# Performance work log

Hardware: AMD Instinct MI355X
Metric: run time of the kernel (lower is better)

## Reference

```python
import jax, jax.numpy as jnp
import numpy as np

S, B, D, A = 8192, 64, 512, 256


def setup_inputs() -> dict:
    key = jax.random.key(0)
    ks = jax.random.split(key, 7)
    return {
        "x": jax.random.normal(ks[0], (S, B, D), dtype=jnp.float32),
        "h": jax.random.normal(ks[1], (1, B, D), dtype=jnp.float32),
        "Wx": jax.random.normal(ks[2], (A, D), dtype=jnp.float32) * (1.0 / np.sqrt(D)),
        "bx": jax.random.normal(ks[3], (A,), dtype=jnp.float32) * 0.01,
        "Wh": jax.random.normal(ks[4], (A, D), dtype=jnp.float32) * (1.0 / np.sqrt(D)),
        "Wt": jax.random.normal(ks[5], (1, A), dtype=jnp.float32) * (1.0 / np.sqrt(A)),
        "bt": jax.random.normal(ks[6], (1,), dtype=jnp.float32) * 0.01,
    }


def reference(x, h, Wx, bx, Wh, Wt, bt):
    # x: (S, B, D) seq-first; h: (1, B, D) hidden state.
    # All Conv1d ops have kernel size 1 -> plain per-position matmuls.
    xb = jnp.transpose(x, (1, 0, 2))               # (B, S, D)
    wx = jnp.einsum('bsd,ad->bas', xb, Wx) + bx[None, :, None]   # (B, A, S)
    h0 = h.transpose(1, 0, 2).reshape(-1, h.shape[-1])           # (B, D)
    wh = h0 @ Wh.T                                                # (B, A)
    # score conv (A -> 1) on tanh(wx + wh), then softmax over seq dim
    score = jnp.einsum('a,bas->bs', Wt[0], jnp.tanh(wx + wh[:, :, None])) + bt[0]  # (B, S)
    attn = jax.nn.softmax(score, axis=-1)                         # (B, S)
    out = jnp.einsum('bs,bsd->bd', attn, xb)                      # (B, D)
    return out
```

## Files before the change

### kernel.cpp

```cpp
#include <hip/hip_runtime.h>


#define S_DIM 8192
#define B_DIM 64
#define D_DIM 512
#define A_DIM 256
#define BM 32
#define NTILES 256

typedef _Float16 half8 __attribute__((ext_vector_type(8)));
typedef float f32x4 __attribute__((ext_vector_type(4)));

__device__ __forceinline__ float tanh_fast(float x) {
  float e = __expf(2.0f * x);
  return 1.0f - 2.0f * __builtin_amdgcn_rcpf(e + 1.0f);
}

__global__ void __launch_bounds__(256)
convw_kernel(const float* __restrict__ Wx, _Float16* __restrict__ Wp) {
  const int idx = (blockIdx.x * 256 + threadIdx.x) * 8;
  const int a = idx >> 9;
  const int k = idx & 511;
  f32x4 va = *(const f32x4*)(Wx + idx);
  f32x4 vb = *(const f32x4*)(Wx + idx + 4);
  half8 hx;
#pragma unroll
  for (int i = 0; i < 4; ++i) { hx[i] = (_Float16)va[i]; hx[4 + i] = (_Float16)vb[i]; }
  const int ta = a >> 4, fr = a & 15;
  const int tk = k >> 5, fg = (k >> 3) & 3;
  *(half8*)(Wp + (ta * 16 + tk) * 512 + (fg * 16 + fr) * 8) = hx;
}

__global__ void __launch_bounds__(256)
whb_kernel(const float* __restrict__ h, const float* __restrict__ Wh,
           const float* __restrict__ bx, float* __restrict__ whb) {
  __shared__ float hs[D_DIM];
  const int b = blockIdx.x, tid = threadIdx.x;
  hs[tid] = h[b * D_DIM + tid];
  hs[tid + 256] = h[b * D_DIM + 256 + tid];
  __syncthreads();
  const int g = tid >> 4, i = tid & 15;
  for (int pass = 0; pass < 16; ++pass) {
    const int a = pass * 16 + g;
    const f32x4* wrow = (const f32x4*)(Wh + (size_t)a * D_DIM);
    float dot = 0.f;
#pragma unroll
    for (int k = 0; k < 8; ++k) {
      f32x4 wv = wrow[i + k * 16];
      f32x4 hv = *(const f32x4*)(hs + (i + k * 16) * 4);
      dot += wv[0] * hv[0] + wv[1] * hv[1] + wv[2] * hv[2] + wv[3] * hv[3];
    }
#pragma unroll
    for (int mask = 1; mask < 16; mask <<= 1) dot += __shfl_xor(dot, mask, 64);
    if (i == 0) whb[b * A_DIM + a] = dot + bx[a];
  }
}

__global__ void __launch_bounds__(256, 4)
paa_main(const float* __restrict__ x, const _Float16* __restrict__ Wp,
         const float* __restrict__ whb, const float* __restrict__ Wt,
         float* __restrict__ m_arr, float* __restrict__ l_arr,
         float* __restrict__ acc_arr) {
  __shared__ _Float16 xs[BM * D_DIM];
  __shared__ float scorep[4 * BM];

  const int tid = threadIdx.x;
  const int lane = tid & 63;
  const int wv = tid >> 6;
  const int b = blockIdx.x;
  const int tile = blockIdx.y;

  const int fr = lane & 15, fg = lane >> 4;
  const int akey = fr & 7;
  const _Float16* wp = Wp + wv * (4 * 16 * 512) + lane * 8;

  float wt_a[4], whb_a[4];
#pragma unroll
  for (int nf = 0; nf < 4; ++nf) {
    wt_a[nf]  = Wt[wv * 64 + nf * 16 + fr];
    whb_a[nf] = whb[b * A_DIM + wv * 64 + nf * 16 + fr];
  }

  const int srow = tid >> 3, sseg = tid & 7;
  const int skey = srow & 7;
  {
    const float* rp = x + ((size_t)(tile * BM + srow) * B_DIM + b) * D_DIM;
    f32x4 sa[4], sb[4];
#pragma unroll
    for (int p = 0; p < 4; ++p) {
      sa[p] = *(const f32x4*)(rp + p * 64 + sseg * 8);
      sb[p] = *(const f32x4*)(rp + p * 64 + sseg * 8 + 4);
    }
#pragma unroll
    for (int p = 0; p < 4; ++p) {
      half8 hx;
#pragma unroll
      for (int j = 0; j < 4; ++j) { hx[j] = (_Float16)sa[p][j]; hx[4 + j] = (_Float16)sb[p][j]; }
      const int ch = p * 8 + sseg;
      *(half8*)(xs + srow * D_DIM + ((ch ^ skey) * 8)) = hx;
    }
#pragma unroll
    for (int p = 0; p < 4; ++p) {
      sa[p] = *(const f32x4*)(rp + (4 + p) * 64 + sseg * 8);
      sb[p] = *(const f32x4*)(rp + (4 + p) * 64 + sseg * 8 + 4);
    }
#pragma unroll
    for (int p = 0; p < 4; ++p) {
      half8 hx;
#pragma unroll
      for (int j = 0; j < 4; ++j) { hx[j] = (_Float16)sa[p][j]; hx[4 + j] = (_Float16)sb[p][j]; }
      const int ch = (4 + p) * 8 + sseg;
      *(half8*)(xs + srow * D_DIM + ((ch ^ skey) * 8)) = hx;
    }
  }
  __syncthreads();

  f32x4 acc[2][4];
#pragma unroll
  for (int mi = 0; mi < 2; ++mi)
#pragma unroll
    for (int nf = 0; nf < 4; ++nf) acc[mi][nf] = (f32x4){0.f, 0.f, 0.f, 0.f};
#pragma unroll
  for (int tk = 0; tk < 16; ++tk) {
    const int slot = ((tk * 4 + fg) ^ akey) * 8;
    half8 af0 = *(const half8*)(xs + (fr) * D_DIM + slot);
    half8 af1 = *(const half8*)(xs + (16 + fr) * D_DIM + slot);
    half8 bf0 = *(const half8*)(wp + (0 * 16 + tk) * 512);
    half8 bf1 = *(const half8*)(wp + (1 * 16 + tk) * 512);
    half8 bf2 = *(const half8*)(wp + (2 * 16 + tk) * 512);
    half8 bf3 = *(const half8*)(wp + (3 * 16 + tk) * 512);
    acc[0][0] = __builtin_amdgcn_mfma_f32_16x16x32_f16(af0, bf0, acc[0][0], 0, 0, 0);
    acc[0][1] = __builtin_amdgcn_mfma_f32_16x16x32_f16(af0, bf1, acc[0][1], 0, 0, 0);
    acc[0][2] = __builtin_amdgcn_mfma_f32_16x16x32_f16(af0, bf2, acc[0][2], 0, 0, 0);
    acc[0][3] = __builtin_amdgcn_mfma_f32_16x16x32_f16(af0, bf3, acc[0][3], 0, 0, 0);
    acc[1][0] = __builtin_amdgcn_mfma_f32_16x16x32_f16(af1, bf0, acc[1][0], 0, 0, 0);
    acc[1][1] = __builtin_amdgcn_mfma_f32_16x16x32_f16(af1, bf1, acc[1][1], 0, 0, 0);
    acc[1][2] = __builtin_amdgcn_mfma_f32_16x16x32_f16(af1, bf2, acc[1][2], 0, 0, 0);
    acc[1][3] = __builtin_amdgcn_mfma_f32_16x16x32_f16(af1, bf3, acc[1][3], 0, 0, 0);
  }

  {
    float part[2][4];
#pragma unroll
    for (int mi = 0; mi < 2; ++mi)
#pragma unroll
      for (int r = 0; r < 4; ++r) part[mi][r] = 0.f;
#pragma unroll
    for (int nf = 0; nf < 4; ++nf)
#pragma unroll
      for (int mi = 0; mi < 2; ++mi)
#pragma unroll
        for (int r = 0; r < 4; ++r)
          part[mi][r] += wt_a[nf] * tanh_fast(acc[mi][nf][r] + whb_a[nf]);
#pragma unroll
    for (int mask = 1; mask < 16; mask <<= 1)
#pragma unroll
      for (int mi = 0; mi < 2; ++mi)
#pragma unroll
        for (int r = 0; r < 4; ++r) part[mi][r] += __shfl_xor(part[mi][r], mask, 64);
    if (fr == 0) {
#pragma unroll
      for (int mi = 0; mi < 2; ++mi)
#pragma unroll
        for (int r = 0; r < 4; ++r)
          scorep[wv * BM + mi * 16 + fg * 4 + r] = part[mi][r];
    }
  }
  __syncthreads();

  const int rl = lane & 31;
  float sv = scorep[rl] + scorep[BM + rl] + scorep[2 * BM + rl] + scorep[3 * BM + rl];
  float m = sv;
#pragma unroll
  for (int mask = 1; mask < 32; mask <<= 1) m = fmaxf(m, __shfl_xor(m, mask, 64));
  float p = __expf(sv - m);
  float lsum = p;
#pragma unroll
  for (int mask = 1; mask < 32; mask <<= 1) lsum += __shfl_xor(lsum, mask, 64);
  if (tid == 0) {
    m_arr[b * NTILES + tile] = m;
    l_arr[b * NTILES + tile] = lsum;
  }

  {
    const int q = lane >> 4;
    const int ch = wv * 16 + (lane & 15);
    float wacc[8];
#pragma unroll
    for (int j = 0; j < 8; ++j) wacc[j] = 0.f;
#pragma unroll
    for (int k = 0; k < 8; ++k) {
      const int row = q * 8 + k;
      const float pr = __shfl(p, row, 64);
      half8 xv = *(const half8*)(xs + row * D_DIM + ((ch ^ (row & 7)) * 8));
#pragma unroll
      for (int j = 0; j < 8; ++j) wacc[j] += pr * (float)xv[j];
    }
#pragma unroll
    for (int j = 0; j < 8; ++j) wacc[j] += __shfl_xor(wacc[j], 16, 64);
#pragma unroll
    for (int j = 0; j < 8; ++j) wacc[j] += __shfl_xor(wacc[j], 32, 64);
    if (lane < 16) {
      float* ob = acc_arr + ((size_t)(b * NTILES + tile)) * D_DIM + ch * 8;
      *(f32x4*)(ob) = (f32x4){wacc[0], wacc[1], wacc[2], wacc[3]};
      *(f32x4*)(ob + 4) = (f32x4){wacc[4], wacc[5], wacc[6], wacc[7]};
    }
  }
}

__global__ void __launch_bounds__(512)
combine_kernel(const float* __restrict__ m_arr, const float* __restrict__ l_arr,
               const float* __restrict__ acc_arr, float* __restrict__ out) {
  __shared__ float ml[NTILES], ls[NTILES], wl[NTILES];
  const int b = blockIdx.x, tid = threadIdx.x;
  if (tid < NTILES) {
    ml[tid] = m_arr[b * NTILES + tid];
    ls[tid] = l_arr[b * NTILES + tid];
  }
  __syncthreads();
  float M = -1e30f;
  for (int i = 0; i < NTILES; ++i) M = fmaxf(M, ml[i]);
  if (tid < NTILES) wl[tid] = __expf(ml[tid] - M);
  __syncthreads();
  float L = 0.f;
  for (int i = 0; i < NTILES; ++i) L += wl[i] * ls[i];
  float sum = 0.f;
  const size_t base = (size_t)b * NTILES * D_DIM + tid;
  for (int i = 0; i < NTILES; ++i) sum += wl[i] * acc_arr[base + (size_t)i * D_DIM];
  out[b * D_DIM + tid] = sum / L;
}

extern "C" void kernel_launch(void* const* d_in, const int* in_sizes, int n_in,
                              void* d_out, int out_size, void* d_ws, size_t ws_size,
                              hipStream_t stream) {
  const float* x = (const float*)d_in[0];
  const float* h = (const float*)d_in[1];
  const float* Wx = (const float*)d_in[2];
  const float* bx = (const float*)d_in[3];
  const float* Wh = (const float*)d_in[4];
  const float* Wt = (const float*)d_in[5];

  char* ws = (char*)d_ws;
  _Float16* Wp = (_Float16*)ws;
  float* whb = (float*)(ws + 262144);
  float* m_arr = (float*)(ws + 262144 + 65536);
  float* l_arr = (float*)(ws + 262144 + 65536 + 65536);
  float* acc_arr = (float*)(ws + 262144 + 3 * 65536);

  hipLaunchKernelGGL(convw_kernel, dim3(64), dim3(256), 0, stream, Wx, Wp);
  hipLaunchKernelGGL(whb_kernel, dim3(B_DIM), dim3(256), 0, stream, h, Wh, bx, whb);
  hipLaunchKernelGGL(paa_main, dim3(B_DIM, NTILES), dim3(256), 0, stream,
                     x, Wp, whb, Wt, m_arr, l_arr, acc_arr);
  hipLaunchKernelGGL(combine_kernel, dim3(B_DIM), dim3(512), 0, stream,
                     m_arr, l_arr, acc_arr, (float*)d_out);
}
```

Baseline: 368.0 us.

## Use 512-thread blocks with 8 waves and register-preloaded weight fragments

Doubles the main kernel's block size to 8 waves. Each wave now owns 32 of the 256 attention channels, and the x-tile load and weighted-sum phases are split across twice as many threads. All of the wave's Wp fragments (32 half8 values) are loaded into registers before the shared-memory sync, so weight fetch overlaps the x staging and the global loads leave the MFMA loop. This targets more memory parallelism and better latency hiding per block, at the cost of higher register pressure under launch_bounds(512, 8) and an extra shuffle stage in the reduction.

```diff
diff --git a/kernel.cpp b/kernel.cpp
--- a/kernel.cpp
+++ b/kernel.cpp
@@ -56,13 +56,13 @@
   }
 }
 
-__global__ void __launch_bounds__(256, 4)
+__global__ void __launch_bounds__(512, 8)
 paa_main(const float* __restrict__ x, const _Float16* __restrict__ Wp,
          const float* __restrict__ whb, const float* __restrict__ Wt,
          float* __restrict__ m_arr, float* __restrict__ l_arr,
          float* __restrict__ acc_arr) {
   __shared__ _Float16 xs[BM * D_DIM];
-  __shared__ float scorep[4 * BM];
+  __shared__ float scorep[8 * BM];
 
   const int tid = threadIdx.x;
   const int lane = tid & 63;
@@ -72,104 +72,90 @@
 
   const int fr = lane & 15, fg = lane >> 4;
   const int akey = fr & 7;
-  const _Float16* wp = Wp + wv * (4 * 16 * 512) + lane * 8;
-
-  float wt_a[4], whb_a[4];
-#pragma unroll
-  for (int nf = 0; nf < 4; ++nf) {
-    wt_a[nf]  = Wt[wv * 64 + nf * 16 + fr];
-    whb_a[nf] = whb[b * A_DIM + wv * 64 + nf * 16 + fr];
-  }
-
-  const int srow = tid >> 3, sseg = tid & 7;
+
+  const int srow = tid >> 4, sseg = tid & 15;
   const int skey = srow & 7;
-  {
-    const float* rp = x + ((size_t)(tile * BM + srow) * B_DIM + b) * D_DIM;
-    f32x4 sa[4], sb[4];
-#pragma unroll
-    for (int p = 0; p < 4; ++p) {
-      sa[p] = *(const f32x4*)(rp + p * 64 + sseg * 8);
-      sb[p] = *(const f32x4*)(rp + p * 64 + sseg * 8 + 4);
-    }
-#pragma unroll
-    for (int p = 0; p < 4; ++p) {
-      half8 hx;
-#pragma unroll
-      for (int j = 0; j < 4; ++j) { hx[j] = (_Float16)sa[p][j]; hx[4 + j] = (_Float16)sb[p][j]; }
-      const int ch = p * 8 + sseg;
-      *(half8*)(xs + srow * D_DIM + ((ch ^ skey) * 8)) = hx;
-    }
-#pragma unroll
-    for (int p = 0; p < 4; ++p) {
-      sa[p] = *(const f32x4*)(rp + (4 + p) * 64 + sseg * 8);
-      sb[p] = *(const f32x4*)(rp + (4 + p) * 64 + sseg * 8 + 4);
-    }
-#pragma unroll
-    for (int p = 0; p < 4; ++p) {
-      half8 hx;
-#pragma unroll
-      for (int j = 0; j < 4; ++j) { hx[j] = (_Float16)sa[p][j]; hx[4 + j] = (_Float16)sb[p][j]; }
-      const int ch = (4 + p) * 8 + sseg;
-      *(half8*)(xs + srow * D_DIM + ((ch ^ skey) * 8)) = hx;
-    }
-  }
-  __syncthreads();
-
-  f32x4 acc[2][4];
-#pragma unroll
-  for (int mi = 0; mi < 2; ++mi)
-#pragma unroll
-    for (int nf = 0; nf < 4; ++nf) acc[mi][nf] = (f32x4){0.f, 0.f, 0.f, 0.f};
+  const float* rp = x + ((size_t)(tile * BM + srow) * B_DIM + b) * D_DIM;
+  f32x4 sa[4], sb[4];
+#pragma unroll
+  for (int c = 0; c < 4; ++c) {
+    sa[c] = *(const f32x4*)(rp + (c * 16 + sseg) * 8);
+    sb[c] = *(const f32x4*)(rp + (c * 16 + sseg) * 8 + 4);
+  }
+
+  half8 wreg[2][16];
+#pragma unroll
+  for (int nf = 0; nf < 2; ++nf)
+#pragma unroll
+    for (int tk = 0; tk < 16; ++tk)
+      wreg[nf][tk] = *(const half8*)(Wp + ((wv * 2 + nf) * 16 + tk) * 512 + lane * 8);
+
+  float wt_a[2], whb_a[2];
+#pragma unroll
+  for (int nf = 0; nf < 2; ++nf) {
+    wt_a[nf]  = Wt[wv * 32 + nf * 16 + fr];
+    whb_a[nf] = whb[b * A_DIM + wv * 32 + nf * 16 + fr];
+  }
+
+#pragma unroll
+  for (int c = 0; c < 4; ++c) {
+    half8 hx;
+#pragma unroll
+    for (int j = 0; j < 4; ++j) { hx[j] = (_Float16)sa[c][j]; hx[4 + j] = (_Float16)sb[c][j]; }
+    const int ch = c * 16 + sseg;
+    *(half8*)(xs + srow * D_DIM + ((ch ^ skey) * 8)) = hx;
+  }
+  __syncthreads();
+
+  f32x4 acc[2][2];
+#pragma unroll
+  for (int mf = 0; mf < 2; ++mf)
+#pragma unroll
+    for (int nf = 0; nf < 2; ++nf) acc[mf][nf] = (f32x4){0.f, 0.f, 0.f, 0.f};
 #pragma unroll
   for (int tk = 0; tk < 16; ++tk) {
     const int slot = ((tk * 4 + fg) ^ akey) * 8;
     half8 af0 = *(const half8*)(xs + (fr) * D_DIM + slot);
     half8 af1 = *(const half8*)(xs + (16 + fr) * D_DIM + slot);
-    half8 bf0 = *(const half8*)(wp + (0 * 16 + tk) * 512);
-    half8 bf1 = *(const half8*)(wp + (1 * 16 + tk) * 512);
-    half8 bf2 = *(const half8*)(wp + (2 * 16 + tk) * 512);
-    half8 bf3 = *(const half8*)(wp + (3 * 16 + tk) * 512);
-    acc[0][0] = __builtin_amdgcn_mfma_f32_16x16x32_f16(af0, bf0, acc[0][0], 0, 0, 0);
-    acc[0][1] = __builtin_amdgcn_mfma_f32_16x16x32_f16(af0, bf1, acc[0][1], 0, 0, 0);
-    acc[0][2] = __builtin_amdgcn_mfma_f32_16x16x32_f16(af0, bf2, acc[0][2], 0, 0, 0);
-    acc[0][3] = __builtin_amdgcn_mfma_f32_16x16x32_f16(af0, bf3, acc[0][3], 0, 0, 0);
-    acc[1][0] = __builtin_amdgcn_mfma_f32_16x16x32_f16(af1, bf0, acc[1][0], 0, 0, 0);
-    acc[1][1] = __builtin_amdgcn_mfma_f32_16x16x32_f16(af1, bf1, acc[1][1], 0, 0, 0);
-    acc[1][2] = __builtin_amdgcn_mfma_f32_16x16x32_f16(af1, bf2, acc[1][2], 0, 0, 0);
-    acc[1][3] = __builtin_amdgcn_mfma_f32_16x16x32_f16(af1, bf3, acc[1][3], 0, 0, 0);
+    acc[0][0] = __builtin_amdgcn_mfma_f32_16x16x32_f16(af0, wreg[0][tk], acc[0][0], 0, 0, 0);
+    acc[0][1] = __builtin_amdgcn_mfma_f32_16x16x32_f16(af0, wreg[1][tk], acc[0][1], 0, 0, 0);
+    acc[1][0] = __builtin_amdgcn_mfma_f32_16x16x32_f16(af1, wreg[0][tk], acc[1][0], 0, 0, 0);
+    acc[1][1] = __builtin_amdgcn_mfma_f32_16x16x32_f16(af1, wreg[1][tk], acc[1][1], 0, 0, 0);
   }
 
   {
     float part[2][4];
 #pragma unroll
-    for (int mi = 0; mi < 2; ++mi)
-#pragma unroll
-      for (int r = 0; r < 4; ++r) part[mi][r] = 0.f;
-#pragma unroll
-    for (int nf = 0; nf < 4; ++nf)
-#pragma unroll
-      for (int mi = 0; mi < 2; ++mi)
+    for (int mf = 0; mf < 2; ++mf)
+#pragma unroll
+      for (int r = 0; r < 4; ++r) part[mf][r] = 0.f;
+#pragma unroll
+    for (int nf = 0; nf < 2; ++nf)
+#pragma unroll
+      for (int mf = 0; mf < 2; ++mf)
 #pragma unroll
         for (int r = 0; r < 4; ++r)
-          part[mi][r] += wt_a[nf] * tanh_fast(acc[mi][nf][r] + whb_a[nf]);
+          part[mf][r] += wt_a[nf] * tanh_fast(acc[mf][nf][r] + whb_a[nf]);
 #pragma unroll
     for (int mask = 1; mask < 16; mask <<= 1)
 #pragma unroll
-      for (int mi = 0; mi < 2; ++mi)
-#pragma unroll
-        for (int r = 0; r < 4; ++r) part[mi][r] += __shfl_xor(part[mi][r], mask, 64);
+      for (int mf = 0; mf < 2; ++mf)
+#pragma unroll
+        for (int r = 0; r < 4; ++r) part[mf][r] += __shfl_xor(part[mf][r], mask, 64);
     if (fr == 0) {
 #pragma unroll
-      for (int mi = 0; mi < 2; ++mi)
+      for (int mf = 0; mf < 2; ++mf)
 #pragma unroll
         for (int r = 0; r < 4; ++r)
-          scorep[wv * BM + mi * 16 + fg * 4 + r] = part[mi][r];
+          scorep[wv * BM + mf * 16 + fg * 4 + r] = part[mf][r];
     }
   }
   __syncthreads();
 
   const int rl = lane & 31;
-  float sv = scorep[rl] + scorep[BM + rl] + scorep[2 * BM + rl] + scorep[3 * BM + rl];
+  float sv = 0.f;
+#pragma unroll
+  for (int w = 0; w < 8; ++w) sv += scorep[w * BM + rl];
   float m = sv;
 #pragma unroll
   for (int mask = 1; mask < 32; mask <<= 1) m = fmaxf(m, __shfl_xor(m, mask, 64));
@@ -183,24 +169,26 @@
   }
 
   {
-    const int q = lane >> 4;
-    const int ch = wv * 16 + (lane & 15);
+    const int q = lane >> 3;
+    const int ch = wv * 8 + (lane & 7);
     float wacc[8];
 #pragma unroll
     for (int j = 0; j < 8; ++j) wacc[j] = 0.f;
 #pragma unroll
-    for (int k = 0; k < 8; ++k) {
-      const int row = q * 8 + k;
+    for (int k = 0; k < 4; ++k) {
+      const int row = q * 4 + k;
       const float pr = __shfl(p, row, 64);
       half8 xv = *(const half8*)(xs + row * D_DIM + ((ch ^ (row & 7)) * 8));
 #pragma unroll
       for (int j = 0; j < 8; ++j) wacc[j] += pr * (float)xv[j];
     }
 #pragma unroll
+    for (int j = 0; j < 8; ++j) wacc[j] += __shfl_xor(wacc[j], 8, 64);
+#pragma unroll
     for (int j = 0; j < 8; ++j) wacc[j] += __shfl_xor(wacc[j], 16, 64);
 #pragma unroll
     for (int j = 0; j < 8; ++j) wacc[j] += __shfl_xor(wacc[j], 32, 64);
-    if (lane < 16) {
+    if (lane < 8) {
       float* ob = acc_arr + ((size_t)(b * NTILES + tile)) * D_DIM + ch * 8;
       *(f32x4*)(ob) = (f32x4){wacc[0], wacc[1], wacc[2], wacc[3]};
       *(f32x4*)(ob + 4) = (f32x4){wacc[4], wacc[5], wacc[6], wacc[7]};
@@ -249,7 +237,7 @@
 
   hipLaunchKernelGGL(convw_kernel, dim3(64), dim3(256), 0, stream, Wx, Wp);
   hipLaunchKernelGGL(whb_kernel, dim3(B_DIM), dim3(256), 0, stream, h, Wh, bx, whb);
-  hipLaunchKernelGGL(paa_main, dim3(B_DIM, NTILES), dim3(256), 0, stream,
+  hipLaunchKernelGGL(paa_main, dim3(B_DIM, NTILES), dim3(512), 0, stream,
                      x, Wp, whb, Wt, m_arr, l_arr, acc_arr);
   hipLaunchKernelGGL(combine_kernel, dim3(B_DIM), dim3(512), 0, stream,
                      m_arr, l_arr, acc_arr, (float*)d_out);
```

Result: slower. 1.467 ms (+298.6%).

## Warp-specialize main kernel into persistent producer/consumer pipeline with double-buffered x tiles

Applied to the files above, without the earlier changes.

Replaces the one-block-per-tile grid with 512 blocks of 384 threads, each walking 32 sequence tiles. Four MFMA waves compute scores while two producer waves load and convert the next x tile into a second LDS buffer and run the softmax-weighted accumulation for the previous tile. The aim is to overlap global loads of x with tensor-core work and to cut per-block launch and setup cost. In exchange it uses about 74 KB of dynamic shared memory per block, so fewer blocks fit per CU. Only two waves now handle all global loads, so memory parallelism could drop.

```diff
diff --git a/kernel.cpp b/kernel.cpp
--- a/kernel.cpp
+++ b/kernel.cpp
@@ -7,9 +7,13 @@
 #define A_DIM 256
 #define BM 32
 #define NTILES 256
+#define TPB 32
+#define NBLK 512
 
 typedef _Float16 half8 __attribute__((ext_vector_type(8)));
 typedef float f32x4 __attribute__((ext_vector_type(4)));
+
+#define SMEM_MAIN (65536 + 1024 + 8192)
 
 __device__ __forceinline__ float tanh_fast(float x) {
   float e = __expf(2.0f * x);
@@ -56,155 +60,241 @@
   }
 }
 
-__global__ void __launch_bounds__(256, 4)
+__global__ void __launch_bounds__(384, 3)
 paa_main(const float* __restrict__ x, const _Float16* __restrict__ Wp,
          const float* __restrict__ whb, const float* __restrict__ Wt,
          float* __restrict__ m_arr, float* __restrict__ l_arr,
          float* __restrict__ acc_arr) {
-  __shared__ _Float16 xs[BM * D_DIM];
-  __shared__ float scorep[4 * BM];
+  extern __shared__ char smem[];
+  _Float16* xs0 = (_Float16*)smem;
+  _Float16* xs1 = (_Float16*)(smem + 32768);
+  float* scorep = (float*)(smem + 65536);
+  float* part   = (float*)(smem + 65536 + 1024);
 
   const int tid = threadIdx.x;
   const int lane = tid & 63;
   const int wv = tid >> 6;
-  const int b = blockIdx.x;
-  const int tile = blockIdx.y;
+  const int b = blockIdx.x & 63;
+  const int sgrp = blockIdx.x >> 6;
+  const int t0 = sgrp * TPB;
 
   const int fr = lane & 15, fg = lane >> 4;
   const int akey = fr & 7;
+
   const _Float16* wp = Wp + wv * (4 * 16 * 512) + lane * 8;
-
   float wt_a[4], whb_a[4];
-#pragma unroll
-  for (int nf = 0; nf < 4; ++nf) {
-    wt_a[nf]  = Wt[wv * 64 + nf * 16 + fr];
-    whb_a[nf] = whb[b * A_DIM + wv * 64 + nf * 16 + fr];
-  }
-
-  const int srow = tid >> 3, sseg = tid & 7;
-  const int skey = srow & 7;
-  {
-    const float* rp = x + ((size_t)(tile * BM + srow) * B_DIM + b) * D_DIM;
+  if (wv < 4) {
+#pragma unroll
+    for (int nf = 0; nf < 4; ++nf) {
+      wt_a[nf]  = Wt[wv * 64 + nf * 16 + fr];
+      whb_a[nf] = whb[b * A_DIM + wv * 64 + nf * 16 + fr];
+    }
+  }
+
+  const int ptid = tid - 256;
+  const int prow = (ptid >= 0) ? (ptid >> 2) : 0;
+  const int quad = (ptid >= 0) ? (ptid & 3) : 0;
+  const int pw = wv - 4;
+
+  auto stage_tile = [&](int tile, _Float16* buf) {
+    const float* rp = x + ((size_t)(tile * BM + prow) * B_DIM + b) * D_DIM;
     f32x4 sa[4], sb[4];
 #pragma unroll
-    for (int p = 0; p < 4; ++p) {
-      sa[p] = *(const f32x4*)(rp + p * 64 + sseg * 8);
-      sb[p] = *(const f32x4*)(rp + p * 64 + sseg * 8 + 4);
-    }
-#pragma unroll
-    for (int p = 0; p < 4; ++p) {
+    for (int c = 0; c < 4; ++c) {
+      sa[c] = *(const f32x4*)(rp + (quad * 16 + c) * 8);
+      sb[c] = *(const f32x4*)(rp + (quad * 16 + c) * 8 + 4);
+    }
+#pragma unroll
+    for (int c = 0; c < 4; ++c) {
       half8 hx;
 #pragma unroll
-      for (int j = 0; j < 4; ++j) { hx[j] = (_Float16)sa[p][j]; hx[4 + j] = (_Float16)sb[p][j]; }
-      const int ch = p * 8 + sseg;
-      *(half8*)(xs + srow * D_DIM + ((ch ^ skey) * 8)) = hx;
-    }
-#pragma unroll
-    for (int p = 0; p < 4; ++p) {
-      sa[p] = *(const f32x4*)(rp + (4 + p) * 64 + sseg * 8);
-      sb[p] = *(const f32x4*)(rp + (4 + p) * 64 + sseg * 8 + 4);
-    }
-#pragma unroll
-    for (int p = 0; p < 4; ++p) {
+      for (int j = 0; j < 4; ++j) { hx[j] = (_Float16)sa[c][j]; hx[4 + j] = (_Float16)sb[c][j]; }
+      const int ch = quad * 16 + c;
+      *(half8*)(buf + prow * D_DIM + ((ch ^ (prow & 7)) * 8)) = hx;
+    }
+#pragma unroll
+    for (int c = 0; c < 4; ++c) {
+      sa[c] = *(const f32x4*)(rp + (quad * 16 + 4 + c) * 8);
+      sb[c] = *(const f32x4*)(rp + (quad * 16 + 4 + c) * 8 + 4);
+    }
+#pragma unroll
+    for (int c = 0; c < 4; ++c) {
       half8 hx;
 #pragma unroll
-      for (int j = 0; j < 4; ++j) { hx[j] = (_Float16)sa[p][j]; hx[4 + j] = (_Float16)sb[p][j]; }
-      const int ch = (4 + p) * 8 + sseg;
-      *(half8*)(xs + srow * D_DIM + ((ch ^ skey) * 8)) = hx;
-    }
-  }
-  __syncthreads();
-
-  f32x4 acc[2][4];
-#pragma unroll
-  for (int mi = 0; mi < 2; ++mi)
-#pragma unroll
-    for (int nf = 0; nf < 4; ++nf) acc[mi][nf] = (f32x4){0.f, 0.f, 0.f, 0.f};
-#pragma unroll
-  for (int tk = 0; tk < 16; ++tk) {
-    const int slot = ((tk * 4 + fg) ^ akey) * 8;
-    half8 af0 = *(const half8*)(xs + (fr) * D_DIM + slot);
-    half8 af1 = *(const half8*)(xs + (16 + fr) * D_DIM + slot);
-    half8 bf0 = *(const half8*)(wp + (0 * 16 + tk) * 512);
-    half8 bf1 = *(const half8*)(wp + (1 * 16 + tk) * 512);
-    half8 bf2 = *(const half8*)(wp + (2 * 16 + tk) * 512);
-    half8 bf3 = *(const half8*)(wp + (3 * 16 + tk) * 512);
-    acc[0][0] = __builtin_amdgcn_mfma_f32_16x16x32_f16(af0, bf0, acc[0][0], 0, 0, 0);
-    acc[0][1] = __builtin_amdgcn_mfma_f32_16x16x32_f16(af0, bf1, acc[0][1], 0, 0, 0);
-    acc[0][2] = __builtin_amdgcn_mfma_f32_16x16x32_f16(af0, bf2, acc[0][2], 0, 0, 0);
-    acc[0][3] = __builtin_amdgcn_mfma_f32_16x16x32_f16(af0, bf3, acc[0][3], 0, 0, 0);
-    acc[1][0] = __builtin_amdgcn_mfma_f32_16x16x32_f16(af1, bf0, acc[1][0], 0, 0, 0);
-    acc[1][1] = __builtin_amdgcn_mfma_f32_16x16x32_f16(af1, bf1, acc[1][1], 0, 0, 0);
-    acc[1][2] = __builtin_amdgcn_mfma_f32_16x16x32_f16(af1, bf2, acc[1][2], 0, 0, 0);
-    acc[1][3] = __builtin_amdgcn_mfma_f32_16x16x32_f16(af1, bf3, acc[1][3], 0, 0, 0);
-  }
-
-  {
-    float part[2][4];
-#pragma unroll
-    for (int mi = 0; mi < 2; ++mi)
-#pragma unroll
-      for (int r = 0; r < 4; ++r) part[mi][r] = 0.f;
-#pragma unroll
-    for (int nf = 0; nf < 4; ++nf)
+      for (int j = 0; j < 4; ++j) { hx[j] = (_Float16)sa[c][j]; hx[4 + j] = (_Float16)sb[c][j]; }
+      const int ch = quad * 16 + 4 + c;
+      *(half8*)(buf + prow * D_DIM + ((ch ^ (prow & 7)) * 8)) = hx;
+    }
+#pragma unroll
+    for (int c = 0; c < 8; ++c) {
+      sa[c & 3] = *(const f32x4*)(rp + (quad * 16 + 8 + c) * 8);
+      sb[c & 3] = *(const f32x4*)(rp + (quad * 16 + 8 + c) * 8 + 4);
+      if ((c & 3) == 3) {
+#pragma unroll
+        for (int cc = 0; cc < 4; ++cc) {
+          half8 hx;
+#pragma unroll
+          for (int j = 0; j < 4; ++j) { hx[j] = (_Float16)sa[cc][j]; hx[4 + j] = (_Float16)sb[cc][j]; }
+          const int ch = quad * 16 + 8 + (c - 3) + cc;
+          *(half8*)(buf + prow * D_DIM + ((ch ^ (prow & 7)) * 8)) = hx;
+        }
+      }
+    }
+  };
+
+  if (wv >= 4) stage_tile(t0, xs0);
+  __syncthreads();
+
+  for (int i = 0; i < TPB; ++i) {
+    const int par = i & 1;
+    _Float16* xcur = par ? xs1 : xs0;
+
+    if (wv < 4) {
+      f32x4 acc[2][4];
 #pragma unroll
       for (int mi = 0; mi < 2; ++mi)
 #pragma unroll
-        for (int r = 0; r < 4; ++r)
-          part[mi][r] += wt_a[nf] * tanh_fast(acc[mi][nf][r] + whb_a[nf]);
-#pragma unroll
-    for (int mask = 1; mask < 16; mask <<= 1)
+        for (int nf = 0; nf < 4; ++nf) acc[mi][nf] = (f32x4){0.f, 0.f, 0.f, 0.f};
+#pragma unroll
+      for (int tk = 0; tk < 16; ++tk) {
+        const int slot = ((tk * 4 + fg) ^ akey) * 8;
+        half8 af0 = *(const half8*)(xcur + (fr) * D_DIM + slot);
+        half8 af1 = *(const half8*)(xcur + (16 + fr) * D_DIM + slot);
+        half8 bf0 = *(const half8*)(wp + (0 * 16 + tk) * 512);
+        half8 bf1 = *(const half8*)(wp + (1 * 16 + tk) * 512);
+        half8 bf2 = *(const half8*)(wp + (2 * 16 + tk) * 512);
+        half8 bf3 = *(const half8*)(wp + (3 * 16 + tk) * 512);
+        acc[0][0] = __builtin_amdgcn_mfma_f32_16x16x32_f16(af0, bf0, acc[0][0], 0, 0, 0);
+        acc[0][1] = __builtin_amdgcn_mfma_f32_16x16x32_f16(af0, bf1, acc[0][1], 0, 0, 0);
+        acc[0][2] = __builtin_amdgcn_mfma_f32_16x16x32_f16(af0, bf2, acc[0][2], 0, 0, 0);
+        acc[0][3] = __builtin_amdgcn_mfma_f32_16x16x32_f16(af0, bf3, acc[0][3], 0, 0, 0);
+        acc[1][0] = __builtin_amdgcn_mfma_f32_16x16x32_f16(af1, bf0, acc[1][0], 0, 0, 0);
+        acc[1][1] = __builtin_amdgcn_mfma_f32_16x16x32_f16(af1, bf1, acc[1][1], 0, 0, 0);
+        acc[1][2] = __builtin_amdgcn_mfma_f32_16x16x32_f16(af1, bf2, acc[1][2], 0, 0, 0);
+        acc[1][3] = __builtin_amdgcn_mfma_f32_16x16x32_f16(af1, bf3, acc[1][3], 0, 0, 0);
+      }
+      float pt[2][4];
 #pragma unroll
       for (int mi = 0; mi < 2; ++mi)
 #pragma unroll
-        for (int r = 0; r < 4; ++r) part[mi][r] += __shfl_xor(part[mi][r], mask, 64);
-    if (fr == 0) {
-#pragma unroll
-      for (int mi = 0; mi < 2; ++mi)
-#pragma unroll
-        for (int r = 0; r < 4; ++r)
-          scorep[wv * BM + mi * 16 + fg * 4 + r] = part[mi][r];
-    }
-  }
-  __syncthreads();
-
-  const int rl = lane & 31;
-  float sv = scorep[rl] + scorep[BM + rl] + scorep[2 * BM + rl] + scorep[3 * BM + rl];
-  float m = sv;
-#pragma unroll
-  for (int mask = 1; mask < 32; mask <<= 1) m = fmaxf(m, __shfl_xor(m, mask, 64));
-  float p = __expf(sv - m);
-  float lsum = p;
-#pragma unroll
-  for (int mask = 1; mask < 32; mask <<= 1) lsum += __shfl_xor(lsum, mask, 64);
-  if (tid == 0) {
-    m_arr[b * NTILES + tile] = m;
-    l_arr[b * NTILES + tile] = lsum;
-  }
-
-  {
-    const int q = lane >> 4;
-    const int ch = wv * 16 + (lane & 15);
-    float wacc[8];
-#pragma unroll
-    for (int j = 0; j < 8; ++j) wacc[j] = 0.f;
-#pragma unroll
-    for (int k = 0; k < 8; ++k) {
-      const int row = q * 8 + k;
-      const float pr = __shfl(p, row, 64);
-      half8 xv = *(const half8*)(xs + row * D_DIM + ((ch ^ (row & 7)) * 8));
-#pragma unroll
-      for (int j = 0; j < 8; ++j) wacc[j] += pr * (float)xv[j];
-    }
-#pragma unroll
-    for (int j = 0; j < 8; ++j) wacc[j] += __shfl_xor(wacc[j], 16, 64);
-#pragma unroll
-    for (int j = 0; j < 8; ++j) wacc[j] += __shfl_xor(wacc[j], 32, 64);
-    if (lane < 16) {
-      float* ob = acc_arr + ((size_t)(b * NTILES + tile)) * D_DIM + ch * 8;
-      *(f32x4*)(ob) = (f32x4){wacc[0], wacc[1], wacc[2], wacc[3]};
-      *(f32x4*)(ob + 4) = (f32x4){wacc[4], wacc[5], wacc[6], wacc[7]};
-    }
+        for (int r = 0; r < 4; ++r) pt[mi][r] = 0.f;
+#pragma unroll
+      for (int nf = 0; nf < 4; ++nf)
+#pragma unroll
+        for (int mi = 0; mi < 2; ++mi)
+#pragma unroll
+          for (int r = 0; r < 4; ++r)
+            pt[mi][r] += wt_a[nf] * tanh_fast(acc[mi][nf][r] + whb_a[nf]);
+#pragma unroll
+      for (int mask = 1; mask < 16; mask <<= 1)
+#pragma unroll
+        for (int mi = 0; mi < 2; ++mi)
+#pragma unroll
+          for (int r = 0; r < 4; ++r) pt[mi][r] += __shfl_xor(pt[mi][r], mask, 64);
+      if (fr == 0) {
+#pragma unroll
+        for (int mi = 0; mi < 2; ++mi)
+#pragma unroll
+          for (int r = 0; r < 4; ++r)
+            scorep[par * 128 + wv * BM + mi * 16 + fg * 4 + r] = pt[mi][r];
+      }
+    } else {
+      const int ppar = par ^ 1;
+      if (i >= 2) {
+        const int c0 = ptid * 4;
+        f32x4 p0 = *(const f32x4*)(part + par * 1024 + c0);
+        f32x4 p1 = *(const f32x4*)(part + par * 1024 + 512 + c0);
+        f32x4 s = {p0[0] + p1[0], p0[1] + p1[1], p0[2] + p1[2], p0[3] + p1[3]};
+        *(f32x4*)(acc_arr + ((size_t)(b * NTILES + t0 + i - 2)) * D_DIM + c0) = s;
+      }
+      if (i >= 1) {
+        _Float16* xprev = ppar ? xs1 : xs0;
+        const int rl = lane & 31;
+        float sv = scorep[ppar * 128 + rl] + scorep[ppar * 128 + 32 + rl]
+                 + scorep[ppar * 128 + 64 + rl] + scorep[ppar * 128 + 96 + rl];
+        float m = sv;
+#pragma unroll
+        for (int mask = 1; mask < 32; mask <<= 1) m = fmaxf(m, __shfl_xor(m, mask, 64));
+        float p = __expf(sv - m);
+        float lsum = p;
+#pragma unroll
+        for (int mask = 1; mask < 32; mask <<= 1) lsum += __shfl_xor(lsum, mask, 64);
+        if (pw == 0 && lane == 0) {
+          m_arr[b * NTILES + t0 + i - 1] = m;
+          l_arr[b * NTILES + t0 + i - 1] = lsum;
+        }
+        float wacc[8];
+#pragma unroll
+        for (int j = 0; j < 8; ++j) wacc[j] = 0.f;
+#pragma unroll
+        for (int k = 0; k < 16; ++k) {
+          const int row = pw * 16 + k;
+          const float pr = __shfl(p, row, 64);
+          half8 xv = *(const half8*)(xprev + row * D_DIM + ((lane ^ (row & 7)) * 8));
+#pragma unroll
+          for (int j = 0; j < 8; ++j) wacc[j] += pr * (float)xv[j];
+        }
+        float* pb = part + ppar * 1024 + pw * 512 + lane * 8;
+        *(f32x4*)(pb) = (f32x4){wacc[0], wacc[1], wacc[2], wacc[3]};
+        *(f32x4*)(pb + 4) = (f32x4){wacc[4], wacc[5], wacc[6], wacc[7]};
+      }
+      if (i + 1 < TPB) {
+        stage_tile(t0 + i + 1, ppar ? xs1 : xs0);
+      }
+    }
+
+    __syncthreads();
+  }
+
+  if (wv >= 4) {
+    const int lpar = (TPB - 1) & 1;
+    {
+      const int c0 = ptid * 4;
+      f32x4 p0 = *(const f32x4*)(part + (lpar ^ 1) * 1024 + c0);
+      f32x4 p1 = *(const f32x4*)(part + (lpar ^ 1) * 1024 + 512 + c0);
+      f32x4 s = {p0[0] + p1[0], p0[1] + p1[1], p0[2] + p1[2], p0[3] + p1[3]};
+      *(f32x4*)(acc_arr + ((size_t)(b * NTILES + t0 + TPB - 2)) * D_DIM + c0) = s;
+    }
+    {
+      _Float16* xprev = lpar ? xs1 : xs0;
+      const int rl = lane & 31;
+      float sv = scorep[lpar * 128 + rl] + scorep[lpar * 128 + 32 + rl]
+               + scorep[lpar * 128 + 64 + rl] + scorep[lpar * 128 + 96 + rl];
+      float m = sv;
+#pragma unroll
+      for (int mask = 1; mask < 32; mask <<= 1) m = fmaxf(m, __shfl_xor(m, mask, 64));
+      float p = __expf(sv - m);
+      float lsum = p;
+#pragma unroll
+      for (int mask = 1; mask < 32; mask <<= 1) lsum += __shfl_xor(lsum, mask, 64);
+      if (pw == 0 && lane == 0) {
+        m_arr[b * NTILES + t0 + TPB - 1] = m;
+        l_arr[b * NTILES + t0 + TPB - 1] = lsum;
+      }
+      float wacc[8];
+#pragma unroll
+      for (int j = 0; j < 8; ++j) wacc[j] = 0.f;
+#pragma unroll
+      for (int k = 0; k < 16; ++k) {
+        const int row = pw * 16 + k;
+        const float pr = __shfl(p, row, 64);
+        half8 xv = *(const half8*)(xprev + row * D_DIM + ((lane ^ (row & 7)) * 8));
+#pragma unroll
+        for (int j = 0; j < 8; ++j) wacc[j] += pr * (float)xv[j];
+      }
+      float* pb = part + lpar * 1024 + pw * 512 + lane * 8;
+      *(f32x4*)(pb) = (f32x4){wacc[0], wacc[1], wacc[2], wacc[3]};
+      *(f32x4*)(pb + 4) = (f32x4){wacc[4], wacc[5], wacc[6], wacc[7]};
+    }
+  }
+  __syncthreads();
+  if (wv >= 4) {
+    const int lpar = (TPB - 1) & 1;
+    const int c0 = ptid * 4;
+    f32x4 p0 = *(const f32x4*)(part + lpar * 1024 + c0);
+    f32x4 p1 = *(const f32x4*)(part + lpar * 1024 + 512 + c0);
+    f32x4 s = {p0[0] + p1[0], p0[1] + p1[1], p0[2] + p1[2], p0[3] + p1[3]};
+    *(f32x4*)(acc_arr + ((size_t)(b * NTILES + t0 + TPB - 1)) * D_DIM + c0) = s;
   }
 }
 
@@ -247,9 +337,12 @@
   float* l_arr = (float*)(ws + 262144 + 65536 + 65536);
   float* acc_arr = (float*)(ws + 262144 + 3 * 65536);
 
+  hipFuncSetAttribute(reinterpret_cast<const void*>(paa_main),
+                      hipFuncAttributeMaxDynamicSharedMemorySize, SMEM_MAIN);
+
   hipLaunchKernelGGL(convw_kernel, dim3(64), dim3(256), 0, stream, Wx, Wp);
   hipLaunchKernelGGL(whb_kernel, dim3(B_DIM), dim3(256), 0, stream, h, Wh, bx, whb);
-  hipLaunchKernelGGL(paa_main, dim3(B_DIM, NTILES), dim3(256), 0, stream,
+  hipLaunchKernelGGL(paa_main, dim3(NBLK), dim3(384), SMEM_MAIN, stream,
                      x, Wp, whb, Wt, m_arr, l_arr, acc_arr);
   hipLaunchKernelGGL(combine_kernel, dim3(B_DIM), dim3(512), 0, stream,
                      m_arr, l_arr, acc_arr, (float*)d_out);
```

After: 1.091 ms. +196.4%, slower.

## Pipeline x tile staging with MFMA via producer/consumer waves in persistent blocks

Applied to the files above, without the earlier changes.

Converts the main kernel into persistent 512-thread blocks that each process 32 sequence tiles for one batch. Four waves compute the MFMA scores while four other waves stage the next tile into a double-buffered LDS region and finish the previous tile's softmax and weighted sum. This aims to overlap global loads with compute and cut launch/prologue overhead. The risk is that with only 512 blocks and half the waves loading, there may be too few loads in flight to saturate HBM bandwidth.

```diff
diff --git a/kernel.cpp b/kernel.cpp
--- a/kernel.cpp
+++ b/kernel.cpp
@@ -7,9 +7,13 @@
 #define A_DIM 256
 #define BM 32
 #define NTILES 256
+#define TPB 32
+#define NBLK 512
 
 typedef _Float16 half8 __attribute__((ext_vector_type(8)));
 typedef float f32x4 __attribute__((ext_vector_type(4)));
+
+#define SMEM_MAIN (65536 + 1024)
 
 __device__ __forceinline__ float tanh_fast(float x) {
   float e = __expf(2.0f * x);
@@ -56,34 +60,42 @@
   }
 }
 
-__global__ void __launch_bounds__(256, 4)
+__global__ void __launch_bounds__(512, 4)
 paa_main(const float* __restrict__ x, const _Float16* __restrict__ Wp,
          const float* __restrict__ whb, const float* __restrict__ Wt,
          float* __restrict__ m_arr, float* __restrict__ l_arr,
          float* __restrict__ acc_arr) {
-  __shared__ _Float16 xs[BM * D_DIM];
-  __shared__ float scorep[4 * BM];
+  extern __shared__ char smem[];
+  _Float16* xs0 = (_Float16*)smem;
+  _Float16* xs1 = (_Float16*)(smem + 32768);
+  float* scorep = (float*)(smem + 65536);
 
   const int tid = threadIdx.x;
   const int lane = tid & 63;
   const int wv = tid >> 6;
-  const int b = blockIdx.x;
-  const int tile = blockIdx.y;
+  const int b = blockIdx.x & 63;
+  const int sgrp = blockIdx.x >> 6;
+  const int t0 = sgrp * TPB;
 
   const int fr = lane & 15, fg = lane >> 4;
   const int akey = fr & 7;
-  const _Float16* wp = Wp + wv * (4 * 16 * 512) + lane * 8;
-
+
+  const _Float16* wp = Wp + (wv & 3) * (4 * 16 * 512) + lane * 8;
   float wt_a[4], whb_a[4];
-#pragma unroll
-  for (int nf = 0; nf < 4; ++nf) {
-    wt_a[nf]  = Wt[wv * 64 + nf * 16 + fr];
-    whb_a[nf] = whb[b * A_DIM + wv * 64 + nf * 16 + fr];
-  }
-
-  const int srow = tid >> 3, sseg = tid & 7;
+  if (wv < 4) {
+#pragma unroll
+    for (int nf = 0; nf < 4; ++nf) {
+      wt_a[nf]  = Wt[wv * 64 + nf * 16 + fr];
+      whb_a[nf] = whb[b * A_DIM + wv * 64 + nf * 16 + fr];
+    }
+  }
+
+  const int ptid = (tid >= 256) ? (tid - 256) : 0;
+  const int srow = ptid >> 3, sseg = ptid & 7;
   const int skey = srow & 7;
-  {
+  const int pw = (wv >= 4) ? (wv - 4) : 0;
+
+  auto stage_tile = [&](int tile, _Float16* buf) {
     const float* rp = x + ((size_t)(tile * BM + srow) * B_DIM + b) * D_DIM;
     f32x4 sa[4], sb[4];
 #pragma unroll
@@ -97,7 +109,7 @@
 #pragma unroll
       for (int j = 0; j < 4; ++j) { hx[j] = (_Float16)sa[p][j]; hx[4 + j] = (_Float16)sb[p][j]; }
       const int ch = p * 8 + sseg;
-      *(half8*)(xs + srow * D_DIM + ((ch ^ skey) * 8)) = hx;
+      *(half8*)(buf + srow * D_DIM + ((ch ^ skey) * 8)) = hx;
     }
 #pragma unroll
     for (int p = 0; p < 4; ++p) {
@@ -110,81 +122,26 @@
 #pragma unroll
       for (int j = 0; j < 4; ++j) { hx[j] = (_Float16)sa[p][j]; hx[4 + j] = (_Float16)sb[p][j]; }
       const int ch = (4 + p) * 8 + sseg;
-      *(half8*)(xs + srow * D_DIM + ((ch ^ skey) * 8)) = hx;
-    }
-  }
-  __syncthreads();
-
-  f32x4 acc[2][4];
-#pragma unroll
-  for (int mi = 0; mi < 2; ++mi)
-#pragma unroll
-    for (int nf = 0; nf < 4; ++nf) acc[mi][nf] = (f32x4){0.f, 0.f, 0.f, 0.f};
-#pragma unroll
-  for (int tk = 0; tk < 16; ++tk) {
-    const int slot = ((tk * 4 + fg) ^ akey) * 8;
-    half8 af0 = *(const half8*)(xs + (fr) * D_DIM + slot);
-    half8 af1 = *(const half8*)(xs + (16 + fr) * D_DIM + slot);
-    half8 bf0 = *(const half8*)(wp + (0 * 16 + tk) * 512);
-    half8 bf1 = *(const half8*)(wp + (1 * 16 + tk) * 512);
-    half8 bf2 = *(const half8*)(wp + (2 * 16 + tk) * 512);
-    half8 bf3 = *(const half8*)(wp + (3 * 16 + tk) * 512);
-    acc[0][0] = __builtin_amdgcn_mfma_f32_16x16x32_f16(af0, bf0, acc[0][0], 0, 0, 0);
-    acc[0][1] = __builtin_amdgcn_mfma_f32_16x16x32_f16(af0, bf1, acc[0][1], 0, 0, 0);
-    acc[0][2] = __builtin_amdgcn_mfma_f32_16x16x32_f16(af0, bf2, acc[0][2], 0, 0, 0);
-    acc[0][3] = __builtin_amdgcn_mfma_f32_16x16x32_f16(af0, bf3, acc[0][3], 0, 0, 0);
-    acc[1][0] = __builtin_amdgcn_mfma_f32_16x16x32_f16(af1, bf0, acc[1][0], 0, 0, 0);
-    acc[1][1] = __builtin_amdgcn_mfma_f32_16x16x32_f16(af1, bf1, acc[1][1], 0, 0, 0);
-    acc[1][2] = __builtin_amdgcn_mfma_f32_16x16x32_f16(af1, bf2, acc[1][2], 0, 0, 0);
-    acc[1][3] = __builtin_amdgcn_mfma_f32_16x16x32_f16(af1, bf3, acc[1][3], 0, 0, 0);
-  }
-
-  {
-    float part[2][4];
-#pragma unroll
-    for (int mi = 0; mi < 2; ++mi)
-#pragma unroll
-      for (int r = 0; r < 4; ++r) part[mi][r] = 0.f;
-#pragma unroll
-    for (int nf = 0; nf < 4; ++nf)
-#pragma unroll
-      for (int mi = 0; mi < 2; ++mi)
-#pragma unroll
-        for (int r = 0; r < 4; ++r)
-          part[mi][r] += wt_a[nf] * tanh_fast(acc[mi][nf][r] + whb_a[nf]);
-#pragma unroll
-    for (int mask = 1; mask < 16; mask <<= 1)
-#pragma unroll
-      for (int mi = 0; mi < 2; ++mi)
-#pragma unroll
-        for (int r = 0; r < 4; ++r) part[mi][r] += __shfl_xor(part[mi][r], mask, 64);
-    if (fr == 0) {
-#pragma unroll
-      for (int mi = 0; mi < 2; ++mi)
-#pragma unroll
-        for (int r = 0; r < 4; ++r)
-          scorep[wv * BM + mi * 16 + fg * 4 + r] = part[mi][r];
-    }
-  }
-  __syncthreads();
-
-  const int rl = lane & 31;
-  float sv = scorep[rl] + scorep[BM + rl] + scorep[2 * BM + rl] + scorep[3 * BM + rl];
-  float m = sv;
-#pragma unroll
-  for (int mask = 1; mask < 32; mask <<= 1) m = fmaxf(m, __shfl_xor(m, mask, 64));
-  float p = __expf(sv - m);
-  float lsum = p;
-#pragma unroll
-  for (int mask = 1; mask < 32; mask <<= 1) lsum += __shfl_xor(lsum, mask, 64);
-  if (tid == 0) {
-    m_arr[b * NTILES + tile] = m;
-    l_arr[b * NTILES + tile] = lsum;
-  }
-
-  {
+      *(half8*)(buf + srow * D_DIM + ((ch ^ skey) * 8)) = hx;
+    }
+  };
+
+  auto finish_tile = [&](int t_idx, const _Float16* xb, const float* sp) {
+    const int rl = lane & 31;
+    float sv = sp[rl] + sp[32 + rl] + sp[64 + rl] + sp[96 + rl];
+    float m = sv;
+#pragma unroll
+    for (int mask = 1; mask < 32; mask <<= 1) m = fmaxf(m, __shfl_xor(m, mask, 64));
+    float p = __expf(sv - m);
+    float lsum = p;
+#pragma unroll
+    for (int mask = 1; mask < 32; mask <<= 1) lsum += __shfl_xor(lsum, mask, 64);
+    if (pw == 0 && lane == 0) {
+      m_arr[b * NTILES + t_idx] = m;
+      l_arr[b * NTILES + t_idx] = lsum;
+    }
     const int q = lane >> 4;
-    const int ch = wv * 16 + (lane & 15);
+    const int ch = pw * 16 + (lane & 15);
     float wacc[8];
 #pragma unroll
     for (int j = 0; j < 8; ++j) wacc[j] = 0.f;
@@ -192,7 +149,7 @@
     for (int k = 0; k < 8; ++k) {
       const int row = q * 8 + k;
       const float pr = __shfl(p, row, 64);
-      half8 xv = *(const half8*)(xs + row * D_DIM + ((ch ^ (row & 7)) * 8));
+      half8 xv = *(const half8*)(xb + row * D_DIM + ((ch ^ (row & 7)) * 8));
 #pragma unroll
       for (int j = 0; j < 8; ++j) wacc[j] += pr * (float)xv[j];
     }
@@ -201,10 +158,104 @@
 #pragma unroll
     for (int j = 0; j < 8; ++j) wacc[j] += __shfl_xor(wacc[j], 32, 64);
     if (lane < 16) {
-      float* ob = acc_arr + ((size_t)(b * NTILES + tile)) * D_DIM + ch * 8;
+      float* ob = acc_arr + ((size_t)(b * NTILES + t_idx)) * D_DIM + ch * 8;
       *(f32x4*)(ob) = (f32x4){wacc[0], wacc[1], wacc[2], wacc[3]};
       *(f32x4*)(ob + 4) = (f32x4){wacc[4], wacc[5], wacc[6], wacc[7]};
     }
+  };
+
+  if (wv >= 4) stage_tile(t0, xs0);
+  __syncthreads();
+
+  for (int i = 0; i < TPB; ++i) {
+    const int par = i & 1;
+    _Float16* xcur = par ? xs1 : xs0;
+    _Float16* xoth = par ? xs0 : xs1;
+
+    f32x4 acc[2][4];
+    if (wv < 4) {
+#pragma unroll
+      for (int mi = 0; mi < 2; ++mi)
+#pragma unroll
+        for (int nf = 0; nf < 4; ++nf) acc[mi][nf] = (f32x4){0.f, 0.f, 0.f, 0.f};
+#pragma unroll
+      for (int tk = 0; tk < 8; ++tk) {
+        const int slot = ((tk * 4 + fg) ^ akey) * 8;
+        half8 af0 = *(const half8*)(xcur + (fr) * D_DIM + slot);
+        half8 af1 = *(const half8*)(xcur + (16 + fr) * D_DIM + slot);
+        half8 bf0 = *(const half8*)(wp + (0 * 16 + tk) * 512);
+        half8 bf1 = *(const half8*)(wp + (1 * 16 + tk) * 512);
+        half8 bf2 = *(const half8*)(wp + (2 * 16 + tk) * 512);
+        half8 bf3 = *(const half8*)(wp + (3 * 16 + tk) * 512);
+        acc[0][0] = __builtin_amdgcn_mfma_f32_16x16x32_f16(af0, bf0, acc[0][0], 0, 0, 0);
+        acc[0][1] = __builtin_amdgcn_mfma_f32_16x16x32_f16(af0, bf1, acc[0][1], 0, 0, 0);
+        acc[0][2] = __builtin_amdgcn_mfma_f32_16x16x32_f16(af0, bf2, acc[0][2], 0, 0, 0);
+        acc[0][3] = __builtin_amdgcn_mfma_f32_16x16x32_f16(af0, bf3, acc[0][3], 0, 0, 0);
+        acc[1][0] = __builtin_amdgcn_mfma_f32_16x16x32_f16(af1, bf0, acc[1][0], 0, 0, 0);
+        acc[1][1] = __builtin_amdgcn_mfma_f32_16x16x32_f16(af1, bf1, acc[1][1], 0, 0, 0);
+        acc[1][2] = __builtin_amdgcn_mfma_f32_16x16x32_f16(af1, bf2, acc[1][2], 0, 0, 0);
+        acc[1][3] = __builtin_amdgcn_mfma_f32_16x16x32_f16(af1, bf3, acc[1][3], 0, 0, 0);
+      }
+    } else if (i >= 1) {
+      finish_tile(t0 + i - 1, xoth, scorep + (par ^ 1) * 128);
+    }
+
+    __syncthreads();
+
+    if (wv < 4) {
+#pragma unroll
+      for (int tk = 8; tk < 16; ++tk) {
+        const int slot = ((tk * 4 + fg) ^ akey) * 8;
+        half8 af0 = *(const half8*)(xcur + (fr) * D_DIM + slot);
+        half8 af1 = *(const half8*)(xcur + (16 + fr) * D_DIM + slot);
+        half8 bf0 = *(const half8*)(wp + (0 * 16 + tk) * 512);
+        half8 bf1 = *(const half8*)(wp + (1 * 16 + tk) * 512);
+        half8 bf2 = *(const half8*)(wp + (2 * 16 + tk) * 512);
+        half8 bf3 = *(const half8*)(wp + (3 * 16 + tk) * 512);
+        acc[0][0] = __builtin_amdgcn_mfma_f32_16x16x32_f16(af0, bf0, acc[0][0], 0, 0, 0);
+        acc[0][1] = __builtin_amdgcn_mfma_f32_16x16x32_f16(af0, bf1, acc[0][1], 0, 0, 0);
+        acc[0][2] = __builtin_amdgcn_mfma_f32_16x16x32_f16(af0, bf2, acc[0][2], 0, 0, 0);
+        acc[0][3] = __builtin_amdgcn_mfma_f32_16x16x32_f16(af0, bf3, acc[0][3], 0, 0, 0);
+        acc[1][0] = __builtin_amdgcn_mfma_f32_16x16x32_f16(af1, bf0, acc[1][0], 0, 0, 0);
+        acc[1][1] = __builtin_amdgcn_mfma_f32_16x16x32_f16(af1, bf1, acc[1][1], 0, 0, 0);
+        acc[1][2] = __builtin_amdgcn_mfma_f32_16x16x32_f16(af1, bf2, acc[1][2], 0, 0, 0);
+        acc[1][3] = __builtin_amdgcn_mfma_f32_16x16x32_f16(af1, bf3, acc[1][3], 0, 0, 0);
+      }
+      float pt[2][4];
+#pragma unroll
+      for (int mi = 0; mi < 2; ++mi)
+#pragma unroll
+        for (int r = 0; r < 4; ++r) pt[mi][r] = 0.f;
+#pragma unroll
+      for (int nf = 0; nf < 4; ++nf)
+#pragma unroll
+        for (int mi = 0; mi < 2; ++mi)
+#pragma unroll
+          for (int r = 0; r < 4; ++r)
+            pt[mi][r] += wt_a[nf] * tanh_fast(acc[mi][nf][r] + whb_a[nf]);
+#pragma unroll
+      for (int mask = 1; mask < 16; mask <<= 1)
+#pragma unroll
+        for (int mi = 0; mi < 2; ++mi)
+#pragma unroll
+          for (int r = 0; r < 4; ++r) pt[mi][r] += __shfl_xor(pt[mi][r], mask, 64);
+      if (fr == 0) {
+#pragma unroll
+        for (int mi = 0; mi < 2; ++mi)
+#pragma unroll
+          for (int r = 0; r < 4; ++r)
+            scorep[par * 128 + wv * BM + mi * 16 + fg * 4 + r] = pt[mi][r];
+      }
+    } else if (i + 1 < TPB) {
+      stage_tile(t0 + i + 1, xoth);
+    }
+
+    __syncthreads();
+  }
+
+  if (wv >= 4) {
+    const int lpar = (TPB - 1) & 1;
+    finish_tile(t0 + TPB - 1, lpar ? xs1 : xs0, scorep + lpar * 128);
   }
 }
 
@@ -247,9 +298,12 @@
   float* l_arr = (float*)(ws + 262144 + 65536 + 65536);
   float* acc_arr = (float*)(ws + 262144 + 3 * 65536);
 
+  hipFuncSetAttribute(reinterpret_cast<const void*>(paa_main),
+                      hipFuncAttributeMaxDynamicSharedMemorySize, SMEM_MAIN);
+
   hipLaunchKernelGGL(convw_kernel, dim3(64), dim3(256), 0, stream, Wx, Wp);
   hipLaunchKernelGGL(whb_kernel, dim3(B_DIM), dim3(256), 0, stream, h, Wh, bx, whb);
-  hipLaunchKernelGGL(paa_main, dim3(B_DIM, NTILES), dim3(256), 0, stream,
+  hipLaunchKernelGGL(paa_main, dim3(NBLK), dim3(512), SMEM_MAIN, stream,
                      x, Wp, whb, Wt, m_arr, l_arr, acc_arr);
   hipLaunchKernelGGL(combine_kernel, dim3(B_DIM), dim3(512), 0, stream,
                      m_arr, l_arr, acc_arr, (float*)d_out);
```

Result: slower. 714.1 us (+94.0%).
